# Kernel tuning notes

Hardware: AMD Instinct MI355X
Metric: run time of the kernel (lower is better)

## Reference

```python
import jax, jax.numpy as jnp
import numpy as np

B, C_IN, C_OUT = 32, 64, 128
K_SIZE, STRIDE, PAD, H = 3, 1, 1, 56
H_OUT = (H + 2 * PAD - K_SIZE) // STRIDE + 1


def setup_inputs() -> dict:
    key = jax.random.key(0)
    kx, kw = jax.random.split(key)
    x = jax.random.normal(kx, (B, C_IN, H, H), dtype=jnp.float32)
    # kaiming_uniform-ish init for K of shape [kh, kw, C_in, C_out]
    fan_in = K_SIZE * C_IN * C_OUT  # torch fan_in for this layout (dim1 * receptive field)
    bound = np.sqrt(6.0 / fan_in).astype(np.float32)
    K = jax.random.uniform(kw, (K_SIZE, K_SIZE, C_IN, C_OUT), dtype=jnp.float32,
                           minval=-bound, maxval=bound)
    return {"x": x, "K": K}


def reference(x, K):
    # Faithful to the torch code INCLUDING its mismatched flatten orders:
    #   patch flattened as (C_in, kh, kw); K flattened as (kh, kw, C_in).
    xp = jnp.pad(x, ((0, 0), (0, 0), (PAD, PAD), (PAD, PAD)))
    end = (H_OUT - 1) * STRIDE + 1
    # patches[b, c, di, dj, i, j] = xp[b, c, i*stride+di, j*stride+dj]
    rows = []
    for di in range(K_SIZE):
        cols = []
        for dj in range(K_SIZE):
            cols.append(xp[:, :, di:di + end:STRIDE, dj:dj + end:STRIDE])  # [B,C,Ho,Wo]
        rows.append(jnp.stack(cols, axis=2))  # [B,C,kw,Ho,Wo]
    patches = jnp.stack(rows, axis=2)  # [B, C, kh, kw, Ho, Wo]
    # flatten patch in (C, kh, kw) order -> [B, Ho, Wo, C*kh*kw]
    p = patches.transpose(0, 4, 5, 1, 2, 3).reshape(B, H_OUT, H_OUT, -1)
    # K flattened in (kh, kw, C) order, exactly as K.view(-1, out_channels)
    Kf = K.reshape(-1, C_OUT)  # [kh*kw*C_in, C_out]
    out = p @ Kf  # [B, Ho, Wo, C_out]
    return out.transpose(0, 3, 1, 2)  # [B, C_out, Ho, Wo]
```

## Files before the change

kernel.cpp:

```cpp
#include <hip/hip_runtime.h>
#include <hip/hip_bf16.h>
#include <stdint.h>


#define B_   32
#define CIN  64
#define COUT 128
#define H_   56
#define HP   58
#define F_   576

typedef __attribute__((ext_vector_type(8))) short bf16x8;
typedef __attribute__((ext_vector_type(4))) float f32x4;

#define XP_ELEMS (B_*HP*HP*CIN)
#define XP_SLACK 4096
#define XP_TOTAL (XP_ELEMS + XP_SLACK)
#define WG_ELEMS (COUT*F_)
#define WS_NEEDED ((size_t)(XP_TOTAL + WG_ELEMS) * 2)

#define NROW   (B_*HP)
#define NWBLK  (WG_ELEMS/256)

#define A_STAGE 45056
#define A_ALLOC 45568
#define LDS_TOT (A_ALLOC + 2*16384)

__global__ __launch_bounds__(256) void prep_all(const float* __restrict__ x,
                                                const float* __restrict__ K,
                                                __hip_bfloat16* __restrict__ xpT,
                                                __hip_bfloat16* __restrict__ WgT) {
  const int id = blockIdx.x;
  const int t  = threadIdx.x;

  if (id > NROW) {
    int n = (id - (NROW + 1))*256 + t;
    int co = n / F_, g = n % F_;
    int di = g / 192, dj = (g % 192) / 64, c = g & 63;
    int f  = c*9 + di*3 + dj;
    int kh = f / 192, kw = (f % 192) / 64, cc = f & 63;
    WgT[n] = __float2bfloat16(K[(((size_t)kh*3 + kw)*CIN + cc)*COUT + co]);
    return;
  }
  if (id == NROW) {
    bf16x8 z = (bf16x8)0;
    for (int idx = t; idx < XP_SLACK/8; idx += 256)
      ((bf16x8*)(xpT + XP_ELEMS))[idx] = z;
    return;
  }

  const int b = id / HP, h = id % HP;
  __hip_bfloat16* orow = xpT + (size_t)(b*HP + h) * HP * CIN;
  if (h == 0 || h == HP-1) {
    bf16x8 z = (bf16x8)0;
    for (int idx = t; idx < HP*CIN/8; idx += 256) ((bf16x8*)orow)[idx] = z;
    return;
  }
  __shared__ __align__(16) float tile[CIN][60];
  const float* xrow = x + ((size_t)(b*CIN)*H_ + (h-1)) * H_;
  for (int idx = t; idx < CIN*(H_/4); idx += 256) {
    int c = idx / 14, w4 = idx % 14;
    f32x4 v = *(const f32x4*)(xrow + (size_t)c*H_*H_ + w4*4);
    *(f32x4*)&tile[c][w4*4] = v;
  }
  __syncthreads();
  for (int idx = t; idx < HP*8; idx += 256) {
    int w = idx >> 3, cg = (idx & 7) * 8;
    __align__(16) __hip_bfloat16 tmp[8];
    if (w == 0 || w == HP-1) {
#pragma unroll
      for (int k2 = 0; k2 < 8; ++k2) tmp[k2] = __float2bfloat16(0.f);
    } else {
#pragma unroll
      for (int k2 = 0; k2 < 8; ++k2) tmp[k2] = __float2bfloat16(tile[cg + k2][w-1]);
    }
    *(bf16x8*)(orow + (size_t)w*CIN + cg) = *(const bf16x8*)tmp;
  }
}

__global__ __launch_bounds__(256, 2) void conv_mfma(
    const __hip_bfloat16* __restrict__ xpT,
    const __hip_bfloat16* __restrict__ WgT,
    float* __restrict__ out) {
  __shared__ __align__(16) char lds[LDS_TOT];
  const int t    = threadIdx.x;
  const int wave = t >> 6;
  const int l    = t & 63;
  const int lr   = l & 15, lq = l >> 4;

  const int bid = blockIdx.x;
  const int swz = (bid & 7) * 56 + (bid >> 3);
  const int bb  = swz / 14;
  const int i0  = (swz % 14) * 4;

  f32x4 acc[4][8];
#pragma unroll
  for (int mi = 0; mi < 4; ++mi)
#pragma unroll
    for (int ni = 0; ni < 8; ++ni) acc[mi][ni] = (f32x4)0.f;

  const char* xb    = (const char*)xpT + (size_t)(bb*HP + i0) * HP * CIN * 2;
  const char* wbase = (const char*)WgT;

#pragma unroll
  for (int s = 0; s < 11; ++s) {
    int o = s*4096 + t*16;
    int m = o >> 7;
    const char* src = xb + ((o & ~127) | ((o & 127) ^ ((m & 7) << 4)));
    __builtin_amdgcn_global_load_lds(
        (const __attribute__((address_space(1))) void*)src,
        (__attribute__((address_space(3))) void*)(lds + s*4096 + wave*1024),
        16, 0, 0);
  }

  auto stageB = [&](int q, int buf) {
    const char* wg = wbase + q*128;
    char* Bb = lds + A_ALLOC + buf*16384;
#pragma unroll
    for (int s = 0; s < 4; ++s) {
      int o  = s*4096 + t*16;
      int co = o >> 7;
      const char* src = wg + (size_t)co*1152 + ((o & 127) ^ ((co & 7) << 4));
      __builtin_amdgcn_global_load_lds(
          (const __attribute__((address_space(1))) void*)src,
          (__attribute__((address_space(3))) void*)(Bb + s*4096 + wave*1024),
          16, 0, 0);
    }
  };

  stageB(0, 0);
  __syncthreads();

#pragma unroll
  for (int q = 0; q < 9; ++q) {
    const int buf = q & 1;
    if (q < 8) stageB(q + 1, buf ^ 1);
    const char* Bb = lds + A_ALLOC + buf*16384;
#pragma unroll
    for (int ks = 0; ks < 2; ++ks) {
      const int kg  = q*64 + ks*32;
      const int di  = kg / 192;
      const int rem = kg - di*192;
      bf16x8 a[4], bfr[8];
#pragma unroll
      for (int mi = 0; mi < 4; ++mi) {
        int r   = (wave + di)*58 + mi*16 + lr;
        int tot = r*128 + rem*2 + lq*16;
        int adr = (tot & ~127) | ((tot & 127) ^ (((tot >> 7) & 7) << 4));
        a[mi] = *(const bf16x8*)(lds + adr);
      }
      const int cb = ks*64 + lq*16;
#pragma unroll
      for (int ni = 0; ni < 8; ++ni) {
        int co = ni*16 + lr;
        bfr[ni] = *(const bf16x8*)(Bb + (((co << 7) | cb) ^ ((co & 7) << 4)));
      }
#pragma unroll
      for (int mi = 0; mi < 4; ++mi)
#pragma unroll
        for (int ni = 0; ni < 8; ++ni)
          acc[mi][ni] = __builtin_amdgcn_mfma_f32_16x16x32_bf16(
              a[mi], bfr[ni], acc[mi][ni], 0, 0, 0);
    }
    __syncthreads();
  }

  const int i = i0 + wave;
#pragma unroll
  for (int mi = 0; mi < 4; ++mi) {
    int j0 = mi*16 + lq*4;
    if (j0 < H_) {
#pragma unroll
      for (int ni = 0; ni < 8; ++ni) {
        int co = ni*16 + lr;
        float* dst = out + (((size_t)(bb*COUT + co))*H_ + i)*H_ + j0;
        *(f32x4*)dst = acc[mi][ni];
      }
    }
  }
}

__global__ __launch_bounds__(256) void conv_naive(const float* __restrict__ x,
                                                  const float* __restrict__ K,
                                                  float* __restrict__ out) {
  int idx = blockIdx.x*256 + threadIdx.x;
  const int total = B_*COUT*H_*H_;
  if (idx >= total) return;
  int j = idx % H_, i = (idx / H_) % H_, co = (idx / (H_*H_)) % COUT, b = idx / (H_*H_*COUT);
  float s = 0.f;
  for (int c = 0; c < CIN; ++c)
    for (int di = 0; di < 3; ++di) {
      int ii = i + di - 1;
      if (ii < 0 || ii >= H_) continue;
      for (int dj = 0; dj < 3; ++dj) {
        int jj = j + dj - 1;
        if (jj < 0 || jj >= H_) continue;
        int f = c*9 + di*3 + dj;
        int kh = f / 192, kw = (f % 192) / 64, cc = f & 63;
        s += x[(((size_t)b*CIN + c)*H_ + ii)*H_ + jj] *
             K[(((size_t)kh*3 + kw)*CIN + cc)*COUT + co];
      }
    }
  out[idx] = s;
}

extern "C" void kernel_launch(void* const* d_in, const int* in_sizes, int n_in,
                              void* d_out, int out_size, void* d_ws, size_t ws_size,
                              hipStream_t stream) {
  const float* x = (const float*)d_in[0];
  const float* K = (const float*)d_in[1];
  float* out = (float*)d_out;
  if (ws_size >= WS_NEEDED) {
    __hip_bfloat16* xpT = (__hip_bfloat16*)d_ws;
    __hip_bfloat16* WgT = xpT + XP_TOTAL;
    prep_all<<<NROW + 1 + NWBLK, 256, 0, stream>>>(x, K, xpT, WgT);
    conv_mfma<<<B_*14, 256, 0, stream>>>(xpT, WgT, out);
  } else {
    conv_naive<<<(B_*COUT*H_*H_ + 255)/256, 256, 0, stream>>>(x, K, out);
  }
}
```

Before: 40.93 us.

## Fuse input padding/transpose/bf16 conversion into the MFMA conv kernel

Removes the separate prep pass that wrote a padded, channel-last bf16 copy of x to global memory. Each conv block now loads its six fp32 input rows directly into a swizzled LDS scratch buffer, double-buffered with the B staging area. It then transposes and converts them to bf16 in the same swizzled A layout the MFMA loop already reads. This saves a global write and read of the padded input, but each row is now loaded by up to three blocks and a serialized prologue with several barriers is added before compute.

```diff
diff --git a/kernel.cpp b/kernel.cpp
--- a/kernel.cpp
+++ b/kernel.cpp
@@ -13,73 +13,25 @@
 typedef __attribute__((ext_vector_type(8))) short bf16x8;
 typedef __attribute__((ext_vector_type(4))) float f32x4;
 
-#define XP_ELEMS (B_*HP*HP*CIN)
-#define XP_SLACK 4096
-#define XP_TOTAL (XP_ELEMS + XP_SLACK)
 #define WG_ELEMS (COUT*F_)
-#define WS_NEEDED ((size_t)(XP_TOTAL + WG_ELEMS) * 2)
-
-#define NROW   (B_*HP)
-#define NWBLK  (WG_ELEMS/256)
-
-#define A_STAGE 45056
+#define WS_NEEDED ((size_t)WG_ELEMS * 2)
+#define NWBLK (WG_ELEMS/256)
+
 #define A_ALLOC 45568
 #define LDS_TOT (A_ALLOC + 2*16384)
 
-__global__ __launch_bounds__(256) void prep_all(const float* __restrict__ x,
-                                                const float* __restrict__ K,
-                                                __hip_bfloat16* __restrict__ xpT,
-                                                __hip_bfloat16* __restrict__ WgT) {
-  const int id = blockIdx.x;
-  const int t  = threadIdx.x;
-
-  if (id > NROW) {
-    int n = (id - (NROW + 1))*256 + t;
-    int co = n / F_, g = n % F_;
-    int di = g / 192, dj = (g % 192) / 64, c = g & 63;
-    int f  = c*9 + di*3 + dj;
-    int kh = f / 192, kw = (f % 192) / 64, cc = f & 63;
-    WgT[n] = __float2bfloat16(K[(((size_t)kh*3 + kw)*CIN + cc)*COUT + co]);
-    return;
-  }
-  if (id == NROW) {
-    bf16x8 z = (bf16x8)0;
-    for (int idx = t; idx < XP_SLACK/8; idx += 256)
-      ((bf16x8*)(xpT + XP_ELEMS))[idx] = z;
-    return;
-  }
-
-  const int b = id / HP, h = id % HP;
-  __hip_bfloat16* orow = xpT + (size_t)(b*HP + h) * HP * CIN;
-  if (h == 0 || h == HP-1) {
-    bf16x8 z = (bf16x8)0;
-    for (int idx = t; idx < HP*CIN/8; idx += 256) ((bf16x8*)orow)[idx] = z;
-    return;
-  }
-  __shared__ __align__(16) float tile[CIN][60];
-  const float* xrow = x + ((size_t)(b*CIN)*H_ + (h-1)) * H_;
-  for (int idx = t; idx < CIN*(H_/4); idx += 256) {
-    int c = idx / 14, w4 = idx % 14;
-    f32x4 v = *(const f32x4*)(xrow + (size_t)c*H_*H_ + w4*4);
-    *(f32x4*)&tile[c][w4*4] = v;
-  }
-  __syncthreads();
-  for (int idx = t; idx < HP*8; idx += 256) {
-    int w = idx >> 3, cg = (idx & 7) * 8;
-    __align__(16) __hip_bfloat16 tmp[8];
-    if (w == 0 || w == HP-1) {
-#pragma unroll
-      for (int k2 = 0; k2 < 8; ++k2) tmp[k2] = __float2bfloat16(0.f);
-    } else {
-#pragma unroll
-      for (int k2 = 0; k2 < 8; ++k2) tmp[k2] = __float2bfloat16(tile[cg + k2][w-1]);
-    }
-    *(bf16x8*)(orow + (size_t)w*CIN + cg) = *(const bf16x8*)tmp;
-  }
-}
-
-__global__ __launch_bounds__(256, 2) void conv_mfma(
-    const __hip_bfloat16* __restrict__ xpT,
+__global__ __launch_bounds__(256) void prep_w(const float* __restrict__ K,
+                                              __hip_bfloat16* __restrict__ WgT) {
+  int n = blockIdx.x*256 + threadIdx.x;
+  int co = n / F_, g = n % F_;
+  int di = g / 192, dj = (g % 192) / 64, c = g & 63;
+  int f  = c*9 + di*3 + dj;
+  int kh = f / 192, kw = (f % 192) / 64, cc = f & 63;
+  WgT[n] = __float2bfloat16(K[(((size_t)kh*3 + kw)*CIN + cc)*COUT + co]);
+}
+
+__global__ __launch_bounds__(256, 2) void conv_fused(
+    const float* __restrict__ x,
     const __hip_bfloat16* __restrict__ WgT,
     float* __restrict__ out) {
   __shared__ __align__(16) char lds[LDS_TOT];
@@ -99,20 +51,47 @@
 #pragma unroll
     for (int ni = 0; ni < 8; ++ni) acc[mi][ni] = (f32x4)0.f;
 
-  const char* xb    = (const char*)xpT + (size_t)(bb*HP + i0) * HP * CIN * 2;
-  const char* wbase = (const char*)WgT;
-
-#pragma unroll
-  for (int s = 0; s < 11; ++s) {
-    int o = s*4096 + t*16;
-    int m = o >> 7;
-    const char* src = xb + ((o & ~127) | ((o & 127) ^ ((m & 7) << 4)));
-    __builtin_amdgcn_global_load_lds(
-        (const __attribute__((address_space(1))) void*)src,
-        (__attribute__((address_space(3))) void*)(lds + s*4096 + wave*1024),
-        16, 0, 0);
-  }
-
+  const float* xb    = x + (size_t)bb*CIN*H_*H_;
+  const char*  wbase = (const char*)WgT;
+  char* s0 = lds + A_ALLOC;
+  char* s1 = s0 + 16384;
+
+  auto phaseA = [&](int r, char* s) {
+    const int h = i0 + r;
+    if (h == 0 || h == HP-1) return;
+    const float* xr = xb + (size_t)(h-1)*H_;
+    for (int idx = t; idx < CIN*14; idx += 256) {
+      int c = idx / 14, w4 = idx % 14;
+      f32x4 v = *(const f32x4*)(xr + (size_t)c*(H_*H_) + w4*4);
+      *(f32x4*)(s + c*256 + (w4 ^ (c & 15))*16) = v;
+    }
+  };
+  auto phaseB = [&](int r, const char* s) {
+    const int h = i0 + r;
+    const bool zrow = (h == 0 || h == HP-1);
+    for (int idx = t; idx < HP*8; idx += 256) {
+      int wp = idx >> 3, cg = (idx & 7) * 8;
+      float v[8];
+      if (zrow || wp == 0 || wp == HP-1) {
+#pragma unroll
+        for (int k2 = 0; k2 < 8; ++k2) v[k2] = 0.f;
+      } else {
+        int w = wp - 1, sl = w >> 2, off = w & 3;
+#pragma unroll
+        for (int k2 = 0; k2 < 8; ++k2) {
+          int c = cg + k2;
+          v[k2] = *(const float*)(s + c*256 + ((sl ^ (c & 15))*16) + off*4);
+        }
+      }
+      __align__(16) __hip_bfloat16 tmp[8];
+#pragma unroll
+      for (int k2 = 0; k2 < 8; ++k2) tmp[k2] = __float2bfloat16(v[k2]);
+      int R   = r*HP + wp;
+      int tot = R*128 + cg*2;
+      int adr = (tot & ~127) | ((tot & 127) ^ ((R & 7) << 4));
+      *(bf16x8*)(lds + adr) = *(const bf16x8*)tmp;
+    }
+  };
   auto stageB = [&](int q, int buf) {
     const char* wg = wbase + q*128;
     char* Bb = lds + A_ALLOC + buf*16384;
@@ -128,8 +107,13 @@
     }
   };
 
-  stageB(0, 0);
-  __syncthreads();
+  phaseA(0, s0);                 __syncthreads();
+  phaseB(0, s0);  phaseA(1, s1); __syncthreads();
+  phaseB(1, s1);  phaseA(2, s0); __syncthreads();
+  phaseB(2, s0);  phaseA(3, s1); __syncthreads();
+  phaseB(3, s1);  phaseA(4, s0); __syncthreads();
+  phaseB(4, s0);  phaseA(5, s1); __syncthreads();
+  phaseB(5, s1);  stageB(0, 0);  __syncthreads();
 
 #pragma unroll
   for (int q = 0; q < 9; ++q) {
@@ -144,7 +128,7 @@
       bf16x8 a[4], bfr[8];
 #pragma unroll
       for (int mi = 0; mi < 4; ++mi) {
-        int r   = (wave + di)*58 + mi*16 + lr;
+        int r   = (wave + di)*HP + mi*16 + lr;
         int tot = r*128 + rem*2 + lq*16;
         int adr = (tot & ~127) | ((tot & 127) ^ (((tot >> 7) & 7) << 4));
         a[mi] = *(const bf16x8*)(lds + adr);
@@ -211,10 +195,9 @@
   const float* K = (const float*)d_in[1];
   float* out = (float*)d_out;
   if (ws_size >= WS_NEEDED) {
-    __hip_bfloat16* xpT = (__hip_bfloat16*)d_ws;
-    __hip_bfloat16* WgT = xpT + XP_TOTAL;
-    prep_all<<<NROW + 1 + NWBLK, 256, 0, stream>>>(x, K, xpT, WgT);
-    conv_mfma<<<B_*14, 256, 0, stream>>>(xpT, WgT, out);
+    __hip_bfloat16* WgT = (__hip_bfloat16*)d_ws;
+    prep_w<<<NWBLK, 256, 0, stream>>>(K, WgT);
+    conv_fused<<<B_*14, 256, 0, stream>>>(x, WgT, out);
   } else {
     conv_naive<<<(B_*COUT*H_*H_ + 255)/256, 256, 0, stream>>>(x, K, out);
   }
```

After: 43.65 us. 1.07x slower.

## Halve B stage size, double pipeline steps, add MFMA priority and swizzled prep tile

Applied to the files above, without the earlier changes.

The conv kernel now stages weights in 32-wide K chunks (8 KB per buffer) over 18 steps instead of 64-wide chunks over 9 steps. This cuts LDS use per block, which may allow more resident blocks per CU, and it wraps the MFMA burst in s_setprio to favour the matrix work. The cost is twice as many barriers. The B layout also loses its XOR swizzle, so a 64-byte row stride may cause LDS bank conflicts on B reads. Separately, the prep kernel's transpose tile gets a rotated layout meant to avoid bank conflicts on the column-wise reads.

```diff
diff --git a/kernel.cpp b/kernel.cpp
--- a/kernel.cpp
+++ b/kernel.cpp
@@ -22,9 +22,8 @@
 #define NROW   (B_*HP)
 #define NWBLK  (WG_ELEMS/256)
 
-#define A_STAGE 45056
 #define A_ALLOC 45568
-#define LDS_TOT (A_ALLOC + 2*16384)
+#define LDS_TOT (A_ALLOC + 2*8192)
 
 __global__ __launch_bounds__(256) void prep_all(const float* __restrict__ x,
                                                 const float* __restrict__ K,
@@ -56,25 +55,29 @@
     for (int idx = t; idx < HP*CIN/8; idx += 256) ((bf16x8*)orow)[idx] = z;
     return;
   }
-  __shared__ __align__(16) float tile[CIN][60];
+  __shared__ __align__(16) float scr[CIN*64];
   const float* xrow = x + ((size_t)(b*CIN)*H_ + (h-1)) * H_;
-  for (int idx = t; idx < CIN*(H_/4); idx += 256) {
+  for (int idx = t; idx < CIN*14; idx += 256) {
     int c = idx / 14, w4 = idx % 14;
-    f32x4 v = *(const f32x4*)(xrow + (size_t)c*H_*H_ + w4*4);
-    *(f32x4*)&tile[c][w4*4] = v;
+    f32x4 v = *(const f32x4*)(xrow + (size_t)c*(H_*H_) + w4*4);
+    *(f32x4*)&scr[c*64 + ((w4 + (c >> 3)) & 15)*4] = v;
   }
   __syncthreads();
   for (int idx = t; idx < HP*8; idx += 256) {
-    int w = idx >> 3, cg = (idx & 7) * 8;
+    int wp = idx >> 3, cg = (idx & 7) * 8;
     __align__(16) __hip_bfloat16 tmp[8];
-    if (w == 0 || w == HP-1) {
+    if (wp == 0 || wp == HP-1) {
 #pragma unroll
       for (int k2 = 0; k2 < 8; ++k2) tmp[k2] = __float2bfloat16(0.f);
     } else {
-#pragma unroll
-      for (int k2 = 0; k2 < 8; ++k2) tmp[k2] = __float2bfloat16(tile[cg + k2][w-1]);
-    }
-    *(bf16x8*)(orow + (size_t)w*CIN + cg) = *(const bf16x8*)tmp;
+      int w = wp - 1, sl = w >> 2, off = w & 3;
+#pragma unroll
+      for (int k2 = 0; k2 < 8; ++k2) {
+        int c = cg + k2;
+        tmp[k2] = __float2bfloat16(scr[c*64 + ((sl + (c >> 3)) & 15)*4 + off]);
+      }
+    }
+    *(bf16x8*)(orow + (size_t)wp*CIN + cg) = *(const bf16x8*)tmp;
   }
 }
 
@@ -113,14 +116,14 @@
         16, 0, 0);
   }
 
-  auto stageB = [&](int q, int buf) {
-    const char* wg = wbase + q*128;
-    char* Bb = lds + A_ALLOC + buf*16384;
-#pragma unroll
-    for (int s = 0; s < 4; ++s) {
+  auto stageBh = [&](int hc, int buf) {
+    const char* wg = wbase + hc*64;
+    char* Bb = lds + A_ALLOC + buf*8192;
+#pragma unroll
+    for (int s = 0; s < 2; ++s) {
       int o  = s*4096 + t*16;
-      int co = o >> 7;
-      const char* src = wg + (size_t)co*1152 + ((o & 127) ^ ((co & 7) << 4));
+      int co = o >> 6;
+      const char* src = wg + (size_t)co*1152 + (o & 63);
       __builtin_amdgcn_global_load_lds(
           (const __attribute__((address_space(1))) void*)src,
           (__attribute__((address_space(3))) void*)(Bb + s*4096 + wave*1024),
@@ -128,40 +131,38 @@
     }
   };
 
-  stageB(0, 0);
+  stageBh(0, 0);
   __syncthreads();
 
 #pragma unroll
-  for (int q = 0; q < 9; ++q) {
-    const int buf = q & 1;
-    if (q < 8) stageB(q + 1, buf ^ 1);
-    const char* Bb = lds + A_ALLOC + buf*16384;
-#pragma unroll
-    for (int ks = 0; ks < 2; ++ks) {
-      const int kg  = q*64 + ks*32;
-      const int di  = kg / 192;
-      const int rem = kg - di*192;
-      bf16x8 a[4], bfr[8];
-#pragma unroll
-      for (int mi = 0; mi < 4; ++mi) {
-        int r   = (wave + di)*58 + mi*16 + lr;
-        int tot = r*128 + rem*2 + lq*16;
-        int adr = (tot & ~127) | ((tot & 127) ^ (((tot >> 7) & 7) << 4));
-        a[mi] = *(const bf16x8*)(lds + adr);
-      }
-      const int cb = ks*64 + lq*16;
-#pragma unroll
-      for (int ni = 0; ni < 8; ++ni) {
-        int co = ni*16 + lr;
-        bfr[ni] = *(const bf16x8*)(Bb + (((co << 7) | cb) ^ ((co & 7) << 4)));
-      }
-#pragma unroll
-      for (int mi = 0; mi < 4; ++mi)
-#pragma unroll
-        for (int ni = 0; ni < 8; ++ni)
-          acc[mi][ni] = __builtin_amdgcn_mfma_f32_16x16x32_bf16(
-              a[mi], bfr[ni], acc[mi][ni], 0, 0, 0);
-    }
+  for (int hc = 0; hc < 18; ++hc) {
+    const int buf = hc & 1;
+    if (hc < 17) stageBh(hc + 1, buf ^ 1);
+    const char* Bb = lds + A_ALLOC + buf*8192;
+    const int kg  = hc*32;
+    const int di  = kg / 192;
+    const int rem = kg - di*192;
+    bf16x8 a[4], bq[8];
+#pragma unroll
+    for (int mi = 0; mi < 4; ++mi) {
+      int r   = (wave + di)*HP + mi*16 + lr;
+      int tot = r*128 + rem*2 + lq*16;
+      int adr = (tot & ~127) | ((tot & 127) ^ (((tot >> 7) & 7) << 4));
+      a[mi] = *(const bf16x8*)(lds + adr);
+    }
+#pragma unroll
+    for (int ni = 0; ni < 8; ++ni) {
+      int co = ni*16 + lr;
+      bq[ni] = *(const bf16x8*)(Bb + co*64 + lq*16);
+    }
+    __builtin_amdgcn_s_setprio(1);
+#pragma unroll
+    for (int mi = 0; mi < 4; ++mi)
+#pragma unroll
+      for (int ni = 0; ni < 8; ++ni)
+        acc[mi][ni] = __builtin_amdgcn_mfma_f32_16x16x32_bf16(
+            a[mi], bq[ni], acc[mi][ni], 0, 0, 0);
+    __builtin_amdgcn_s_setprio(0);
     __syncthreads();
   }
 
```

Result: faster. 39.41 us (-3.7%).
